# Performance work log

Hardware: AMD Instinct MI355X
Metric: run time of the kernel (lower is better)

Reference implementation:

```python
import jax, jax.numpy as jnp
import numpy as np

N_WORDS, MAX_CHARS = 32768, 16
WORD_DIM, CHAR_DIM, HIDDEN = 256, 64, 256
VOCAB = 256


def setup_inputs() -> dict:
    key = jax.random.key(0)
    ks = jax.random.split(key, 10)
    char_indices = jax.random.randint(ks[0], (N_WORDS, MAX_CHARS), 0, VOCAB)
    char_lengths = jax.random.randint(ks[1], (N_WORDS,), 1, MAX_CHARS + 1)
    word_emb = jax.random.normal(ks[2], (N_WORDS, WORD_DIM), dtype=jnp.float32)
    s = 0.05
    E_char = jax.random.normal(ks[3], (VOCAB, CHAR_DIM), dtype=jnp.float32) * s
    W_ih = jax.random.normal(ks[4], (4 * HIDDEN, CHAR_DIM), dtype=jnp.float32) * s
    W_hh = jax.random.normal(ks[5], (4 * HIDDEN, HIDDEN), dtype=jnp.float32) * s
    b_ih = jax.random.normal(ks[6], (4 * HIDDEN,), dtype=jnp.float32) * s
    b_hh = jax.random.normal(ks[7], (4 * HIDDEN,), dtype=jnp.float32) * s
    W_lin = jax.random.normal(ks[8], (WORD_DIM, WORD_DIM + HIDDEN), dtype=jnp.float32) * s
    b_lin = jax.random.normal(ks[9], (WORD_DIM,), dtype=jnp.float32) * s
    return dict(char_indices=char_indices, char_lengths=char_lengths,
                word_emb=word_emb, E_char=E_char, W_ih=W_ih, W_hh=W_hh,
                b_ih=b_ih, b_hh=b_hh, W_lin=W_lin, b_lin=b_lin)


def _lstm_last_hidden(x, lengths, W_ih, W_hh, b_ih, b_hh):
    # x: [N, T, E]; returns final hidden h at position length-1 per row.
    N, T, _ = x.shape
    H = W_hh.shape[1]
    x_proj = jnp.einsum('nte,ge->ntg', x, W_ih) + (b_ih + b_hh)  # [N, T, 4H]
    x_proj = jnp.transpose(x_proj, (1, 0, 2))                    # time-major [T, N, 4H]

    def step(carry, inp):
        h, c = carry
        xg, t = inp
        gates = xg + h @ W_hh.T
        i, f, g, o = jnp.split(gates, 4, axis=-1)
        i, f, o = jax.nn.sigmoid(i), jax.nn.sigmoid(f), jax.nn.sigmoid(o)
        g = jnp.tanh(g)
        c_new = f * c + i * g
        h_new = o * jnp.tanh(c_new)
        mask = (t < lengths)[:, None]  # freeze state past each word's length
        h = jnp.where(mask, h_new, h)
        c = jnp.where(mask, c_new, c)
        return (h, c), None

    h0 = jnp.zeros((N, H), dtype=x.dtype)
    c0 = jnp.zeros((N, H), dtype=x.dtype)
    (h, _), _ = jax.lax.scan(step, (h0, c0), (x_proj, jnp.arange(T)))
    return h


def reference(char_indices, char_lengths, word_emb, E_char, W_ih, W_hh,
              b_ih, b_hh, W_lin, b_lin):
    char_embedded = E_char[char_indices]                        # [N, T, E]
    h = _lstm_last_hidden(char_embedded, char_lengths, W_ih, W_hh, b_ih, b_hh)
    combined = jnp.concatenate([word_emb, h], axis=-1)          # [N, WORD+H]
    return jax.nn.relu(combined @ W_lin.T + b_lin)              # [N, WORD]
```

## Files before the change

### kernel.cpp

```cpp
#include <hip/hip_runtime.h>


#define NW 32768

typedef __attribute__((ext_vector_type(8))) short short8;
typedef __attribute__((ext_vector_type(4))) float f32x4;
typedef __attribute__((ext_vector_type(4))) int i32x4;

#define MFMA16(a,b,c) __builtin_amdgcn_mfma_f32_16x16x32_bf16(a,b,c,0,0,0)
#define MFMAI8(a,b,c) __builtin_amdgcn_mfma_i32_16x16x32_i8(a,b,c,0,0,0)

#define O_ORDER 0
#define O_SLEN  131072
#define O_WPK   262144
#define O_USTP  589824
#define O_BIAS  593920
#define O_CHT   598016
#define O_WLIN  614400

__device__ inline unsigned short f2b(float f) {
  unsigned u = __builtin_bit_cast(unsigned, f);
  u = u + 0x7fffu + ((u >> 16) & 1u);
  return (unsigned short)(u >> 16);
}
__device__ inline float fsigm(float x) {
  float e = __builtin_amdgcn_exp2f(-1.44269504f * x);
  return __builtin_amdgcn_rcpf(1.0f + e);
}
__device__ inline float ftanh(float x) {
  float e = __builtin_amdgcn_exp2f(2.88539008f * x);
  return 1.0f - 2.0f * __builtin_amdgcn_rcpf(e + 1.0f);
}

__global__ void k_prep0(const float* __restrict__ wih, const float* __restrict__ whh,
                        const float* __restrict__ bih, const float* __restrict__ bhh,
                        const float* __restrict__ ech, unsigned char* __restrict__ ws) {
  int i = blockIdx.x * 256 + threadIdx.x;
  if (i < 1024) {
    float mx = 0.f;
    for (int k = 0; k < 64; ++k)  mx = fmaxf(mx, fabsf(wih[i * 64 + k]) * 0.25f);
    for (int k = 0; k < 256; ++k) mx = fmaxf(mx, fabsf(whh[i * 256 + k]));
    ((float*)(ws + O_USTP))[i] = mx / (127.f * 127.f);
    ((float*)(ws + O_BIAS))[i] = bih[i] + bhh[i];
    return;
  }
  int j = i - 1024;
  if (j < 16384) {
    float v = 508.f * ech[j];
    int q = (int)__builtin_rintf(v);
    q = q < -127 ? -127 : (q > 127 ? 127 : q);
    ((signed char*)(ws + O_CHT))[j] = (signed char)q;
  }
}

__global__ void k_prep1(const float* __restrict__ wih, const float* __restrict__ whh,
                        const float* __restrict__ wlin, unsigned char* __restrict__ ws) {
  int i = blockIdx.x * 256 + threadIdx.x;
  if (i < 327680) {
    int j = i & 7, lane = (i >> 3) & 63, t2 = i >> 9;
    int nt = t2 & 7, u2 = t2 >> 3;
    int kb = u2 % 10, w = u2 / 10;
    int n = (nt >> 1) * 256 + w * 32 + (nt & 1) * 16 + (lane & 15);
    int k = kb * 32 + (lane >> 4) * 8 + j;
    float v = (k < 64) ? wih[n * 64 + k] * 0.25f : whh[n * 256 + (k - 64)];
    float ustep = ((const float*)(ws + O_USTP))[n] * 127.f;
    float qf = (ustep > 0.f) ? v / ustep : 0.f;
    int q = (int)__builtin_rintf(qf);
    q = q < -127 ? -127 : (q > 127 ? 127 : q);
    ((signed char*)(ws + O_WPK))[i] = (signed char)q;
    return;
  }
  int i2 = i - 327680;
  if (i2 < 131072) {
    int j = i2 & 7, lane = (i2 >> 3) & 63, t3 = i2 >> 9;
    int kf = t3 & 15, nn = t3 >> 4;
    int n = (nn >> 2) * 64 + (nn & 3) * 16 + (lane & 15);
    int k = kf * 32 + (lane >> 4) * 8 + j;
    ((unsigned short*)(ws + O_WLIN))[i2] = f2b(wlin[n * 512 + k]);
  }
}

__global__ void k_sort(const int* __restrict__ lens, unsigned char* __restrict__ ws) {
  __shared__ unsigned hist[16], pos[16];
  int tid = threadIdx.x;
  if (tid < 16) hist[tid] = 0;
  __syncthreads();
  for (int w = tid; w < NW; w += 1024) {
    int l = lens[w]; l = l < 1 ? 1 : (l > 16 ? 16 : l);
    atomicAdd(&hist[l - 1], 1u);
  }
  __syncthreads();
  if (tid == 0) {
    unsigned acc = 0;
    for (int l = 0; l < 16; ++l) { pos[l] = acc; acc += hist[l]; }
  }
  __syncthreads();
  int* order = (int*)(ws + O_ORDER);
  int* slenp = (int*)(ws + O_SLEN);
  for (int w = tid; w < NW; w += 1024) {
    int l = lens[w]; l = l < 1 ? 1 : (l > 16 ? 16 : l);
    unsigned p = atomicAdd(&pos[l - 1], 1u);
    order[p] = w; slenp[p] = l;
  }
}

__global__ __launch_bounds__(512, 2) void k_main(
    const int* __restrict__ cidx, const float* __restrict__ wemb,
    const float* __restrict__ blin, float* __restrict__ outp,
    const unsigned char* __restrict__ ws) {
  extern __shared__ signed char smem[];
  signed char (*WL)[8][8][64][8] = (signed char (*)[8][8][64][8])smem;
  signed char (*Xb)[10][64][8] = (signed char (*)[10][64][8])(smem + 98304);
  signed char (*CT)[64] = (signed char (*)[64])(smem + 98304 + 20480);
  int (*CW)[16] = (int (*)[16])(smem + 98304 + 20480 + 16384);

  const int tid = threadIdx.x, b = blockIdx.x;
  const int w = tid >> 6, lane = tid & 63;
  const int q = lane >> 4, l15 = lane & 15;

  const int* order = (const int*)(ws + O_ORDER);
  const int* slen  = (const int*)(ws + O_SLEN);
  const signed char* wpk = (const signed char*)(ws + O_WPK);
  const float* upt = (const float*)(ws + O_USTP);
  const float* bsg = (const float*)(ws + O_BIAS);
  const unsigned short* wlin = (const unsigned short*)(ws + O_WLIN);

  {
    long* d = (long*)&CT[0][0];
    const long* s = (const long*)(ws + O_CHT);
    #pragma unroll
    for (int ii = 0; ii < 4; ++ii) d[tid + 512 * ii] = s[tid + 512 * ii];
  }
  long wreg[7][8];
  #pragma unroll
  for (int kb = 0; kb < 7; ++kb)
    #pragma unroll
    for (int nt = 0; nt < 8; ++nt)
      wreg[kb][nt] = *(const long*)(wpk + (((w * 10 + kb) * 8 + nt) * 64 + lane) * 8);
  #pragma unroll
  for (int c = 0; c < 24; ++c) {
    int kb = c >> 3, nt = c & 7;
    *(long*)&WL[kb][w][nt][lane][0] =
        *(const long*)(wpk + (((w * 10 + 7 + kb) * 8 + nt) * 64 + lane) * 8);
  }
  float uq[8], bq[8];
  #pragma unroll
  for (int nt = 0; nt < 8; ++nt) {
    int n = (nt >> 1) * 256 + w * 32 + (nt & 1) * 16 + l15;
    uq[nt] = upt[n]; bq[nt] = bsg[n];
  }
  const int mh = w >> 2, nw = w & 3;
  float blv[4];
  #pragma unroll
  for (int nt = 0; nt < 4; ++nt) blv[nt] = blin[nw * 64 + nt * 16 + l15];

  for (int sl = 0; sl < 2; ++sl) {
    const int s = sl ? (511 - b) : b;
    const int base = 64 * s;
    __syncthreads();

    {
      long* p = (long*)&Xb[0][0][0][0];
      #pragma unroll
      for (int ii = 0; ii < 4; ++ii) {
        int idx = tid + 512 * ii;
        int mt = idx >> 9, rem = idx & 511;
        p[mt * 640 + 128 + rem] = 0L;
      }
    }
    if (tid < 256) {
      int m = tid >> 2, part = tid & 3;
      int wid = order[base + m];
      *(i32x4*)&CW[m][part * 4] = *(const i32x4*)(cidx + wid * 16 + part * 4);
    }
    int tmax[4]; unsigned lenpk[4];
    #pragma unroll
    for (int mt = 0; mt < 4; ++mt) {
      int pbm = base + 16 * mt;
      tmax[mt] = slen[pbm + 15];
      unsigned l0 = (unsigned)slen[pbm + q * 4 + 0];
      unsigned l1 = (unsigned)slen[pbm + q * 4 + 1];
      unsigned l2 = (unsigned)slen[pbm + q * 4 + 2];
      unsigned l3 = (unsigned)slen[pbm + q * 4 + 3];
      lenpk[mt] = l0 | (l1 << 8) | (l2 << 16) | (l3 << 24);
    }
    const int Tm = tmax[3];
    __syncthreads();
    {
      int m = tid >> 3, c = tid & 7, kb = c >> 2, kq = c & 3;
      int ch = CW[m][0] & 255;
      *(long*)&Xb[m >> 4][kb][(m & 15) + 16 * kq][0] = *(const long*)&CT[ch][kb * 32 + kq * 8];
    }
    __syncthreads();

    float creg[4][2][4];
    #pragma unroll
    for (int mt = 0; mt < 4; ++mt)
      #pragma unroll
      for (int hs = 0; hs < 2; ++hs)
        #pragma unroll
        for (int r = 0; r < 4; ++r) creg[mt][hs][r] = 0.f;
    unsigned hpack[4][2];

    for (int t = 0; t < Tm; ++t) {
      bool actm[4];
      actm[0] = t < tmax[0]; actm[1] = t < tmax[1];
      actm[2] = t < tmax[2]; actm[3] = true;

      #pragma unroll
      for (int mt = 0; mt < 4; ++mt) {
        if (!actm[mt]) continue;
        i32x4 acc[8];
        #pragma unroll
        for (int nt = 0; nt < 8; ++nt) acc[nt] = (i32x4)0;
        #pragma unroll
        for (int kb = 0; kb < 7; ++kb) {
          long A = *(const long*)&Xb[mt][kb][lane][0];
          #pragma unroll
          for (int nt = 0; nt < 8; ++nt) acc[nt] = MFMAI8(A, wreg[kb][nt], acc[nt]);
        }
        #pragma unroll
        for (int kb = 7; kb < 10; ++kb) {
          long A = *(const long*)&Xb[mt][kb][lane][0];
          #pragma unroll
          for (int nt = 0; nt < 8; ++nt) {
            long Bv = *(const long*)&WL[kb - 7][w][nt][lane][0];
            acc[nt] = MFMAI8(A, Bv, acc[nt]);
          }
        }
        #pragma unroll
        for (int hs = 0; hs < 2; ++hs) {
          unsigned hp = 0;
          #pragma unroll
          for (int r = 0; r < 4; ++r) {
            float gi = (float)acc[0 + hs][r] * uq[0 + hs] + bq[0 + hs];
            float gf = (float)acc[2 + hs][r] * uq[2 + hs] + bq[2 + hs];
            float gg = (float)acc[4 + hs][r] * uq[4 + hs] + bq[4 + hs];
            float go = (float)acc[6 + hs][r] * uq[6 + hs] + bq[6 + hs];
            float si = fsigm(gi), sf = fsigm(gf);
            float sg = ftanh(gg), so = fsigm(go);
            float cold = creg[mt][hs][r];
            float cn = sf * cold + si * sg;
            float hn = so * ftanh(cn);
            int lene = (int)((lenpk[mt] >> (8 * r)) & 255u);
            creg[mt][hs][r] = (t < lene) ? cn : cold;
            int hq = (int)__builtin_rintf(127.f * hn);
            hq = hq < -127 ? -127 : (hq > 127 ? 127 : hq);
            hp |= ((unsigned)hq & 255u) << (8 * r);
          }
          hpack[mt][hs] = hp;
        }
      }
      __syncthreads();

      #pragma unroll
      for (int mt = 0; mt < 4; ++mt) {
        if (!actm[mt]) continue;
        #pragma unroll
        for (int hs = 0; hs < 2; ++hs) {
          int kqp = hs * 2 + (l15 >> 3);
          #pragma unroll
          for (int r = 0; r < 4; ++r) {
            int lene = (int)((lenpk[mt] >> (8 * r)) & 255u);
            if (t < lene)
              Xb[mt][2 + w][(q * 4 + r) + 16 * kqp][l15 & 7] =
                  (signed char)((hpack[mt][hs] >> (8 * r)) & 255u);
          }
        }
      }
      if (t + 1 < Tm) {
        int m = tid >> 3, c = tid & 7, kb = c >> 2, kq = c & 3;
        int ch = CW[m][t + 1] & 255;
        *(long*)&Xb[m >> 4][kb][(m & 15) + 16 * kq][0] = *(const long*)&CT[ch][kb * 32 + kq * 8];
      }
      __syncthreads();
    }

    int widA[2];
    #pragma unroll
    for (int mi = 0; mi < 2; ++mi) widA[mi] = order[base + (2 * mh + mi) * 16 + l15];
    f32x4 fac[2][4];
    #pragma unroll
    for (int mi = 0; mi < 2; ++mi)
      #pragma unroll
      for (int nt = 0; nt < 4; ++nt) fac[mi][nt] = 0.0f;

    #pragma unroll
    for (int kf = 0; kf < 16; ++kf) {
      short8 Bn[4];
      #pragma unroll
      for (int nt = 0; nt < 4; ++nt)
        Bn[nt] = ((const short8*)wlin)[((nw * 4 + nt) * 16 + kf) * 64 + lane];
      short8 Am[2];
      #pragma unroll
      for (int mi = 0; mi < 2; ++mi) {
        if (kf < 8) {
          const f32x4* pa = (const f32x4*)(wemb + widA[mi] * 256 + kf * 32 + q * 8);
          f32x4 f0 = pa[0], f1 = pa[1];
          short8 A;
          A[0] = (short)f2b(f0[0]); A[1] = (short)f2b(f0[1]);
          A[2] = (short)f2b(f0[2]); A[3] = (short)f2b(f0[3]);
          A[4] = (short)f2b(f1[0]); A[5] = (short)f2b(f1[1]);
          A[6] = (short)f2b(f1[2]); A[7] = (short)f2b(f1[3]);
          Am[mi] = A;
        } else {
          long ch = *(const long*)&Xb[2 * mh + mi][kf - 6][lane][0];
          short8 A;
          #pragma unroll
          for (int j = 0; j < 8; ++j) {
            int v = (int)(signed char)((ch >> (8 * j)) & 255);
            A[j] = (short)f2b((float)v * (1.f / 127.f));
          }
          Am[mi] = A;
        }
      }
      #pragma unroll
      for (int mi = 0; mi < 2; ++mi)
        #pragma unroll
        for (int nt = 0; nt < 4; ++nt)
          fac[mi][nt] = MFMA16(Am[mi], Bn[nt], fac[mi][nt]);
    }
    #pragma unroll
    for (int mi = 0; mi < 2; ++mi) {
      #pragma unroll
      for (int r = 0; r < 4; ++r) {
        int wid = order[base + (2 * mh + mi) * 16 + q * 4 + r];
        float* po = outp + wid * 256 + nw * 64 + l15;
        #pragma unroll
        for (int nt = 0; nt < 4; ++nt) {
          float v = fac[mi][nt][r] + blv[nt];
          po[nt * 16] = v > 0.f ? v : 0.f;
        }
      }
    }
  }
}

extern "C" void kernel_launch(void* const* d_in, const int* in_sizes, int n_in,
                              void* d_out, int out_size, void* d_ws, size_t ws_size,
                              hipStream_t stream) {
  const int*   cidx = (const int*)d_in[0];
  const int*   clen = (const int*)d_in[1];
  const float* wemb = (const float*)d_in[2];
  const float* ech  = (const float*)d_in[3];
  const float* wih  = (const float*)d_in[4];
  const float* whh  = (const float*)d_in[5];
  const float* bih  = (const float*)d_in[6];
  const float* bhh  = (const float*)d_in[7];
  const float* wlin = (const float*)d_in[8];
  const float* blin = (const float*)d_in[9];
  float* outp = (float*)d_out;
  unsigned char* ws = (unsigned char*)d_ws;

  k_prep0<<<68, 256, 0, stream>>>(wih, whh, bih, bhh, ech, ws);
  k_prep1<<<1792, 256, 0, stream>>>(wih, whh, wlin, ws);
  k_sort<<<1, 1024, 0, stream>>>(clen, ws);
  k_main<<<256, 512, 139264, stream>>>(cidx, wemb, blin, outp, ws);
}
```

Measured before the change: 456.0 us.

## Precompute per-character input gate projections and double-buffer hidden state in LSTM

Replaces the per-step int8 input-projection MFMAs with a precomputed fp32 table of W_ih·E_char + biases indexed by character, so the recurrence only multiplies the hidden state (K=256, all weights held in registers, no LDS weight tiles). The hidden-state LDS buffer is double-buffered, which removes one of the two barriers per timestep, and frozen rows keep their old h in registers. The single-block sort becomes a multi-block histogram/scan/scatter. This adds kernel launches and gathers from a 1 MB projection table each step, and the input projection is now exact fp32 instead of quantized.

```diff
diff --git a/kernel.cpp b/kernel.cpp
--- a/kernel.cpp
+++ b/kernel.cpp
@@ -13,10 +13,11 @@
 #define O_ORDER 0
 #define O_SLEN  131072
 #define O_WPK   262144
-#define O_USTP  589824
-#define O_BIAS  593920
-#define O_CHT   598016
-#define O_WLIN  614400
+#define O_USTP  524288
+#define O_WLIN  528384
+#define O_PX    790528
+#define O_BH    1839104
+#define O_BASE  1847296
 
 __device__ inline unsigned short f2b(float f) {
   unsigned u = __builtin_bit_cast(unsigned, f);
@@ -32,37 +33,29 @@
   return 1.0f - 2.0f * __builtin_amdgcn_rcpf(e + 1.0f);
 }
 
-__global__ void k_prep0(const float* __restrict__ wih, const float* __restrict__ whh,
-                        const float* __restrict__ bih, const float* __restrict__ bhh,
-                        const float* __restrict__ ech, unsigned char* __restrict__ ws) {
+__global__ void k_prep0(const float* __restrict__ whh, unsigned char* __restrict__ ws) {
   int i = blockIdx.x * 256 + threadIdx.x;
-  if (i < 1024) {
-    float mx = 0.f;
-    for (int k = 0; k < 64; ++k)  mx = fmaxf(mx, fabsf(wih[i * 64 + k]) * 0.25f);
-    for (int k = 0; k < 256; ++k) mx = fmaxf(mx, fabsf(whh[i * 256 + k]));
-    ((float*)(ws + O_USTP))[i] = mx / (127.f * 127.f);
-    ((float*)(ws + O_BIAS))[i] = bih[i] + bhh[i];
-    return;
-  }
-  int j = i - 1024;
-  if (j < 16384) {
-    float v = 508.f * ech[j];
-    int q = (int)__builtin_rintf(v);
-    q = q < -127 ? -127 : (q > 127 ? 127 : q);
-    ((signed char*)(ws + O_CHT))[j] = (signed char)q;
-  }
-}
-
-__global__ void k_prep1(const float* __restrict__ wih, const float* __restrict__ whh,
-                        const float* __restrict__ wlin, unsigned char* __restrict__ ws) {
+  const f32x4* r4 = (const f32x4*)(whh + i * 256);
+  float mx = 0.f;
+  #pragma unroll 8
+  for (int k4 = 0; k4 < 64; ++k4) {
+    f32x4 v = r4[k4];
+    mx = fmaxf(mx, fmaxf(fmaxf(fabsf(v[0]), fabsf(v[1])),
+                         fmaxf(fabsf(v[2]), fabsf(v[3]))));
+  }
+  ((float*)(ws + O_USTP))[i] = mx / (127.f * 127.f);
+}
+
+__global__ void k_prep1(const float* __restrict__ whh, const float* __restrict__ wlin,
+                        unsigned char* __restrict__ ws) {
   int i = blockIdx.x * 256 + threadIdx.x;
-  if (i < 327680) {
+  if (i < 262144) {
     int j = i & 7, lane = (i >> 3) & 63, t2 = i >> 9;
     int nt = t2 & 7, u2 = t2 >> 3;
-    int kb = u2 % 10, w = u2 / 10;
+    int kb = u2 & 7, w = u2 >> 3;
     int n = (nt >> 1) * 256 + w * 32 + (nt & 1) * 16 + (lane & 15);
     int k = kb * 32 + (lane >> 4) * 8 + j;
-    float v = (k < 64) ? wih[n * 64 + k] * 0.25f : whh[n * 256 + (k - 64)];
+    float v = whh[n * 256 + k];
     float ustep = ((const float*)(ws + O_USTP))[n] * 127.f;
     float qf = (ustep > 0.f) ? v / ustep : 0.f;
     int q = (int)__builtin_rintf(qf);
@@ -70,8 +63,8 @@
     ((signed char*)(ws + O_WPK))[i] = (signed char)q;
     return;
   }
-  int i2 = i - 327680;
-  if (i2 < 131072) {
+  int i2 = i - 262144;
+  {
     int j = i2 & 7, lane = (i2 >> 3) & 63, t3 = i2 >> 9;
     int kf = t3 & 15, nn = t3 >> 4;
     int n = (nn >> 2) * 64 + (nn & 3) * 16 + (lane & 15);
@@ -80,39 +73,72 @@
   }
 }
 
-__global__ void k_sort(const int* __restrict__ lens, unsigned char* __restrict__ ws) {
-  __shared__ unsigned hist[16], pos[16];
-  int tid = threadIdx.x;
-  if (tid < 16) hist[tid] = 0;
-  __syncthreads();
-  for (int w = tid; w < NW; w += 1024) {
-    int l = lens[w]; l = l < 1 ? 1 : (l > 16 ? 16 : l);
-    atomicAdd(&hist[l - 1], 1u);
-  }
-  __syncthreads();
-  if (tid == 0) {
-    unsigned acc = 0;
-    for (int l = 0; l < 16; ++l) { pos[l] = acc; acc += hist[l]; }
-  }
-  __syncthreads();
-  int* order = (int*)(ws + O_ORDER);
-  int* slenp = (int*)(ws + O_SLEN);
-  for (int w = tid; w < NW; w += 1024) {
-    int l = lens[w]; l = l < 1 ? 1 : (l > 16 ? 16 : l);
-    unsigned p = atomicAdd(&pos[l - 1], 1u);
-    order[p] = w; slenp[p] = l;
-  }
+__global__ void k_prep2(const float* __restrict__ wih, const float* __restrict__ ech,
+                        const float* __restrict__ bih, const float* __restrict__ bhh,
+                        unsigned char* __restrict__ ws) {
+  int id = blockIdx.x * 256 + threadIdx.x;
+  int c = id >> 10, n = id & 1023;
+  const f32x4* w4 = (const f32x4*)(wih + n * 64);
+  const f32x4* e4 = (const f32x4*)(ech + c * 64);
+  float acc = bih[n] + bhh[n];
+  #pragma unroll
+  for (int k4 = 0; k4 < 16; ++k4) {
+    f32x4 a = w4[k4], e = e4[k4];
+    acc += a[0] * e[0] + a[1] * e[1] + a[2] * e[2] + a[3] * e[3];
+  }
+  ((float*)(ws + O_PX))[((c << 8) + (n & 255)) * 4 + (n >> 8)] = acc;
+}
+
+__global__ void k_hist(const int* __restrict__ lens, unsigned char* __restrict__ ws) {
+  __shared__ int h[16];
+  int t = threadIdx.x, b = blockIdx.x;
+  if (t < 16) h[t] = 0;
+  __syncthreads();
+  int wid = b * 256 + t;
+  int l = lens[wid]; l = l < 1 ? 1 : (l > 16 ? 16 : l);
+  atomicAdd(&h[l - 1], 1);
+  __syncthreads();
+  if (t < 16) ((int*)(ws + O_BH))[b * 16 + t] = h[t];
+}
+
+__global__ void k_scan(unsigned char* __restrict__ ws) {
+  __shared__ int tot[16], g[16];
+  int t = threadIdx.x;
+  const int* bh = (const int*)(ws + O_BH);
+  int* base = (int*)(ws + O_BASE);
+  if (t < 16) {
+    int s = 0;
+    for (int b = 0; b < 128; ++b) s += bh[b * 16 + t];
+    tot[t] = s;
+  }
+  __syncthreads();
+  if (t == 0) { int a = 0; for (int i = 0; i < 16; ++i) { g[i] = a; a += tot[i]; } }
+  __syncthreads();
+  if (t < 16) {
+    int run = g[t];
+    for (int b = 0; b < 128; ++b) { base[b * 16 + t] = run; run += bh[b * 16 + t]; }
+  }
+}
+
+__global__ void k_scatter(const int* __restrict__ lens, unsigned char* __restrict__ ws) {
+  __shared__ int cnt[16];
+  int t = threadIdx.x, b = blockIdx.x;
+  if (t < 16) cnt[t] = 0;
+  __syncthreads();
+  int wid = b * 256 + t;
+  int l = lens[wid]; l = l < 1 ? 1 : (l > 16 ? 16 : l);
+  int rank = atomicAdd(&cnt[l - 1], 1);
+  int p = ((const int*)(ws + O_BASE))[b * 16 + (l - 1)] + rank;
+  ((int*)(ws + O_ORDER))[p] = wid;
+  ((int*)(ws + O_SLEN))[p] = l;
 }
 
 __global__ __launch_bounds__(512, 2) void k_main(
     const int* __restrict__ cidx, const float* __restrict__ wemb,
     const float* __restrict__ blin, float* __restrict__ outp,
     const unsigned char* __restrict__ ws) {
-  extern __shared__ signed char smem[];
-  signed char (*WL)[8][8][64][8] = (signed char (*)[8][8][64][8])smem;
-  signed char (*Xb)[10][64][8] = (signed char (*)[10][64][8])(smem + 98304);
-  signed char (*CT)[64] = (signed char (*)[64])(smem + 98304 + 20480);
-  int (*CW)[16] = (int (*)[16])(smem + 98304 + 20480 + 16384);
+  __shared__ signed char Xb[2][4][8][64][8];
+  __shared__ int CW[64][16];
 
   const int tid = threadIdx.x, b = blockIdx.x;
   const int w = tid >> 6, lane = tid & 63;
@@ -122,33 +148,23 @@
   const int* slen  = (const int*)(ws + O_SLEN);
   const signed char* wpk = (const signed char*)(ws + O_WPK);
   const float* upt = (const float*)(ws + O_USTP);
-  const float* bsg = (const float*)(ws + O_BIAS);
   const unsigned short* wlin = (const unsigned short*)(ws + O_WLIN);
-
-  {
-    long* d = (long*)&CT[0][0];
-    const long* s = (const long*)(ws + O_CHT);
-    #pragma unroll
-    for (int ii = 0; ii < 4; ++ii) d[tid + 512 * ii] = s[tid + 512 * ii];
-  }
-  long wreg[7][8];
+  const float* pxt = (const float*)(ws + O_PX);
+
+  long wreg[8][8];
   #pragma unroll
-  for (int kb = 0; kb < 7; ++kb)
+  for (int kb = 0; kb < 8; ++kb)
     #pragma unroll
     for (int nt = 0; nt < 8; ++nt)
-      wreg[kb][nt] = *(const long*)(wpk + (((w * 10 + kb) * 8 + nt) * 64 + lane) * 8);
-  #pragma unroll
-  for (int c = 0; c < 24; ++c) {
-    int kb = c >> 3, nt = c & 7;
-    *(long*)&WL[kb][w][nt][lane][0] =
-        *(const long*)(wpk + (((w * 10 + 7 + kb) * 8 + nt) * 64 + lane) * 8);
-  }
-  float uq[8], bq[8];
+      wreg[kb][nt] = *(const long*)(wpk + (((w * 8 + kb) * 8 + nt) * 64 + lane) * 8);
+
+  float uq[8];
   #pragma unroll
   for (int nt = 0; nt < 8; ++nt) {
     int n = (nt >> 1) * 256 + w * 32 + (nt & 1) * 16 + l15;
-    uq[nt] = upt[n]; bq[nt] = bsg[n];
-  }
+    uq[nt] = upt[n];
+  }
+  const int hd0 = w * 32 + l15;
   const int mh = w >> 2, nw = w & 3;
   float blv[4];
   #pragma unroll
@@ -158,15 +174,10 @@
     const int s = sl ? (511 - b) : b;
     const int base = 64 * s;
     __syncthreads();
-
     {
-      long* p = (long*)&Xb[0][0][0][0];
-      #pragma unroll
-      for (int ii = 0; ii < 4; ++ii) {
-        int idx = tid + 512 * ii;
-        int mt = idx >> 9, rem = idx & 511;
-        p[mt * 640 + 128 + rem] = 0L;
-      }
+      long* p = (long*)&Xb[0][0][0][0][0];
+      #pragma unroll
+      for (int ii = 0; ii < 4; ++ii) p[tid + 512 * ii] = 0L;
     }
     if (tid < 256) {
       int m = tid >> 2, part = tid & 3;
@@ -186,99 +197,85 @@
     }
     const int Tm = tmax[3];
     __syncthreads();
-    {
-      int m = tid >> 3, c = tid & 7, kb = c >> 2, kq = c & 3;
-      int ch = CW[m][0] & 255;
-      *(long*)&Xb[m >> 4][kb][(m & 15) + 16 * kq][0] = *(const long*)&CT[ch][kb * 32 + kq * 8];
-    }
-    __syncthreads();
 
     float creg[4][2][4];
+    unsigned hreg[4][2];
     #pragma unroll
     for (int mt = 0; mt < 4; ++mt)
       #pragma unroll
-      for (int hs = 0; hs < 2; ++hs)
+      for (int hs = 0; hs < 2; ++hs) {
+        hreg[mt][hs] = 0u;
         #pragma unroll
         for (int r = 0; r < 4; ++r) creg[mt][hs][r] = 0.f;
-    unsigned hpack[4][2];
+      }
 
     for (int t = 0; t < Tm; ++t) {
-      bool actm[4];
-      actm[0] = t < tmax[0]; actm[1] = t < tmax[1];
-      actm[2] = t < tmax[2]; actm[3] = true;
-
+      const int rd = t & 1, wb = rd ^ 1;
       #pragma unroll
       for (int mt = 0; mt < 4; ++mt) {
-        if (!actm[mt]) continue;
-        i32x4 acc[8];
-        #pragma unroll
-        for (int nt = 0; nt < 8; ++nt) acc[nt] = (i32x4)0;
-        #pragma unroll
-        for (int kb = 0; kb < 7; ++kb) {
-          long A = *(const long*)&Xb[mt][kb][lane][0];
-          #pragma unroll
-          for (int nt = 0; nt < 8; ++nt) acc[nt] = MFMAI8(A, wreg[kb][nt], acc[nt]);
-        }
-        #pragma unroll
-        for (int kb = 7; kb < 10; ++kb) {
-          long A = *(const long*)&Xb[mt][kb][lane][0];
-          #pragma unroll
-          for (int nt = 0; nt < 8; ++nt) {
-            long Bv = *(const long*)&WL[kb - 7][w][nt][lane][0];
-            acc[nt] = MFMAI8(A, Bv, acc[nt]);
+        if (mt != 3 && t >= tmax[mt]) continue;
+        int cc[4];
+        #pragma unroll
+        for (int r = 0; r < 4; ++r) cc[r] = CW[mt * 16 + q * 4 + r][t] & 255;
+        #pragma unroll
+        for (int hs = 0; hs < 2; ++hs) {
+          f32x4 pxv[4];
+          #pragma unroll
+          for (int r = 0; r < 4; ++r)
+            pxv[r] = *(const f32x4*)&pxt[((cc[r] << 8) + hd0 + hs * 16) * 4];
+          i32x4 a0 = (i32x4)0, a1 = (i32x4)0, a2 = (i32x4)0, a3 = (i32x4)0;
+          #pragma unroll
+          for (int kb = 0; kb < 8; ++kb) {
+            long A = *(const long*)&Xb[rd][mt][kb][lane][0];
+            a0 = MFMAI8(A, wreg[kb][0 + hs], a0);
+            a1 = MFMAI8(A, wreg[kb][2 + hs], a1);
+            a2 = MFMAI8(A, wreg[kb][4 + hs], a2);
+            a3 = MFMAI8(A, wreg[kb][6 + hs], a3);
           }
-        }
-        #pragma unroll
-        for (int hs = 0; hs < 2; ++hs) {
           unsigned hp = 0;
           #pragma unroll
           for (int r = 0; r < 4; ++r) {
-            float gi = (float)acc[0 + hs][r] * uq[0 + hs] + bq[0 + hs];
-            float gf = (float)acc[2 + hs][r] * uq[2 + hs] + bq[2 + hs];
-            float gg = (float)acc[4 + hs][r] * uq[4 + hs] + bq[4 + hs];
-            float go = (float)acc[6 + hs][r] * uq[6 + hs] + bq[6 + hs];
+            float gi = (float)a0[r] * uq[0 + hs] + pxv[r][0];
+            float gf = (float)a1[r] * uq[2 + hs] + pxv[r][1];
+            float gg = (float)a2[r] * uq[4 + hs] + pxv[r][2];
+            float go = (float)a3[r] * uq[6 + hs] + pxv[r][3];
             float si = fsigm(gi), sf = fsigm(gf);
             float sg = ftanh(gg), so = fsigm(go);
             float cold = creg[mt][hs][r];
             float cn = sf * cold + si * sg;
             float hn = so * ftanh(cn);
             int lene = (int)((lenpk[mt] >> (8 * r)) & 255u);
-            creg[mt][hs][r] = (t < lene) ? cn : cold;
+            bool live = t < lene;
+            creg[mt][hs][r] = live ? cn : cold;
             int hq = (int)__builtin_rintf(127.f * hn);
-            hq = hq < -127 ? -127 : (hq > 127 ? 127 : hq);
-            hp |= ((unsigned)hq & 255u) << (8 * r);
+            unsigned ob = (hreg[mt][hs] >> (8 * r)) & 255u;
+            unsigned nb = live ? ((unsigned)hq & 255u) : ob;
+            hp |= nb << (8 * r);
           }
-          hpack[mt][hs] = hp;
+          hreg[mt][hs] = hp;
         }
       }
+
+      #pragma unroll
+      for (int mt = 0; mt < 4; ++mt) {
+        if (mt != 3 && t >= tmax[mt]) continue;
+        #pragma unroll
+        for (int hs = 0; hs < 2; ++hs) {
+          int row16 = 16 * (hs * 2 + (l15 >> 3));
+          #pragma unroll
+          for (int r = 0; r < 4; ++r)
+            Xb[wb][mt][w][(q * 4 + r) + row16][l15 & 7] =
+                (signed char)((hreg[mt][hs] >> (8 * r)) & 255u);
+        }
+      }
       __syncthreads();
-
-      #pragma unroll
-      for (int mt = 0; mt < 4; ++mt) {
-        if (!actm[mt]) continue;
-        #pragma unroll
-        for (int hs = 0; hs < 2; ++hs) {
-          int kqp = hs * 2 + (l15 >> 3);
-          #pragma unroll
-          for (int r = 0; r < 4; ++r) {
-            int lene = (int)((lenpk[mt] >> (8 * r)) & 255u);
-            if (t < lene)
-              Xb[mt][2 + w][(q * 4 + r) + 16 * kqp][l15 & 7] =
-                  (signed char)((hpack[mt][hs] >> (8 * r)) & 255u);
-          }
-        }
-      }
-      if (t + 1 < Tm) {
-        int m = tid >> 3, c = tid & 7, kb = c >> 2, kq = c & 3;
-        int ch = CW[m][t + 1] & 255;
-        *(long*)&Xb[m >> 4][kb][(m & 15) + 16 * kq][0] = *(const long*)&CT[ch][kb * 32 + kq * 8];
-      }
-      __syncthreads();
     }
 
     int widA[2];
     #pragma unroll
     for (int mi = 0; mi < 2; ++mi) widA[mi] = order[base + (2 * mh + mi) * 16 + l15];
+    const int tb0 = (mh ? tmax[2] : tmax[0]) & 1;
+    const int tb1 = (mh ? tmax[3] : tmax[1]) & 1;
     f32x4 fac[2][4];
     #pragma unroll
     for (int mi = 0; mi < 2; ++mi)
@@ -304,7 +301,9 @@
           A[6] = (short)f2b(f1[2]); A[7] = (short)f2b(f1[3]);
           Am[mi] = A;
         } else {
-          long ch = *(const long*)&Xb[2 * mh + mi][kf - 6][lane][0];
+          int mtv = 2 * mh + mi;
+          int tb = mi ? tb1 : tb0;
+          long ch = *(const long*)&Xb[tb][mtv][kf - 8][lane][0];
           short8 A;
           #pragma unroll
           for (int j = 0; j < 8; ++j) {
@@ -352,8 +351,11 @@
   float* outp = (float*)d_out;
   unsigned char* ws = (unsigned char*)d_ws;
 
-  k_prep0<<<68, 256, 0, stream>>>(wih, whh, bih, bhh, ech, ws);
-  k_prep1<<<1792, 256, 0, stream>>>(wih, whh, wlin, ws);
-  k_sort<<<1, 1024, 0, stream>>>(clen, ws);
-  k_main<<<256, 512, 139264, stream>>>(cidx, wemb, blin, outp, ws);
-}
+  k_prep0<<<4, 256, 0, stream>>>(whh, ws);
+  k_prep1<<<1536, 256, 0, stream>>>(whh, wlin, ws);
+  k_prep2<<<1024, 256, 0, stream>>>(wih, ech, bih, bhh, ws);
+  k_hist<<<128, 256, 0, stream>>>(clen, ws);
+  k_scan<<<1, 64, 0, stream>>>(ws);
+  k_scatter<<<128, 256, 0, stream>>>(clen, ws);
+  k_main<<<256, 512, 0, stream>>>(cidx, wemb, blin, outp, ws);
+}
```

New measurement: 410.1 us. -10.1%, faster.
